# Performance work log

Measured on AMD Instinct MI355X. Metric: run time of the kernel, lower is better.

Reference implementation:

```python
import jax, jax.numpy as jnp
import numpy as np

N_EMBD = 384
HEAD_SIZE = 64
BLOCK_SIZE = 256

def setup_inputs() -> dict:
    key = jax.random.key(0)
    kx, kk, kq, kv = jax.random.split(key, 4)
    bound = 1.0 / np.sqrt(N_EMBD)  # torch nn.Linear default init
    return {
        "x": jax.random.normal(kx, (512, 256, N_EMBD), dtype=jnp.float32),
        "Wk": jax.random.uniform(kk, (N_EMBD, HEAD_SIZE), jnp.float32, -bound, bound),
        "Wq": jax.random.uniform(kq, (N_EMBD, HEAD_SIZE), jnp.float32, -bound, bound),
        "Wv": jax.random.uniform(kv, (N_EMBD, HEAD_SIZE), jnp.float32, -bound, bound),
    }

def reference(x, Wk, Wq, Wv):
    # x: [B, T, C]; single causal self-attention head (eval mode: dropout off)
    B, T, C = x.shape
    k = jnp.einsum('btc,ch->bth', x, Wk)   # [B, T, H]
    q = jnp.einsum('btc,ch->bth', x, Wq)
    v = jnp.einsum('btc,ch->bth', x, Wv)
    scale = 1.0 / jnp.sqrt(jnp.asarray(k.shape[-1], dtype=x.dtype))
    wei = jnp.einsum('bth,bsh->bts', q, k) * scale  # [B, T, T]
    causal = jnp.tril(jnp.ones((T, T), dtype=bool))
    wei = jnp.where(causal, wei, -jnp.inf)
    wei = jax.nn.softmax(wei, axis=-1)
    return jnp.einsum('bts,bsh->bth', wei, v)  # [B, T, H]
```

## Files before the change

### kernel.cpp

```cpp
#include <hip/hip_runtime.h>

#define T_DIM 256
#define C_DIM 384
#define H_DIM 64

typedef __attribute__((ext_vector_type(4))) float f32x4;
typedef __attribute__((ext_vector_type(8))) short bf16x8;
typedef unsigned short u16;

__device__ __forceinline__ u16 f2b(float f) {
  unsigned u = __float_as_uint(f);
  u = (u + 0x7FFFu + ((u >> 16) & 1u)) >> 16;
  return (u16)u;
}
__device__ __forceinline__ unsigned pkbf(float a, float b) {
  unsigned r;
  asm("v_cvt_pk_bf16_f32 %0, %1, %2" : "=v"(r) : "v"(a), "v"(b));
  return r;
}

__device__ __forceinline__ int sw64(int r, int c)  { return r * 64  + (c ^ ((r & 7) << 3)); }
__device__ __forceinline__ int sw256(int h, int t) { return h * 256 + (t ^ ((h & 7) << 3)); }
__device__ __forceinline__ int sw32(int r, int c)  { return r * 32  + (c ^ (((r >> 1) & 3) << 3)); }

__global__ __launch_bounds__(1024, 4)
void head_fused(const float* __restrict__ x,
                const float* __restrict__ Wk,
                const float* __restrict__ Wq,
                const float* __restrict__ Wv,
                float* __restrict__ out)
{
  __shared__ u16 sh[32768];
  u16* xs  = sh;
  u16* wsT = sh + 8192;
  u16* ks  = sh;
  u16* vT  = sh + 16384;

  const int tid  = threadIdx.x;
  const int wv   = tid >> 6;
  const int lane = tid & 63;
  const int g    = lane >> 4;
  const int lr   = lane & 15;
  const int b    = blockIdx.x;

  const float* xb = x + (size_t)b * (T_DIM * C_DIM);

  int xr[2], xc[2];
#pragma unroll
  for (int it = 0; it < 2; ++it) {
    int idx = tid + it * 1024;
    xr[it] = idx >> 3;
    xc[it] = (idx & 7) * 4;
  }
  int wrow[2], wcc[2];
  const float* wsrc[2];
  bool wok[2];
#pragma unroll
  for (int it = 0; it < 2; ++it) {
    int idx = tid + it * 1024;
    wok[it] = (idx < 1536);
    int q   = (idx >> 5) & 63;
    int cc  = idx & 31;
    int seg = q >> 4;
    int hq  = q & 15;
    wrow[it] = seg * 64 + hq * 4;
    wcc[it]  = cc;
    wsrc[it] = ((seg == 0) ? Wq : (seg == 1) ? Wk : Wv) + hq * 4;
  }

  f32x4 acc[12];
#pragma unroll
  for (int nj = 0; nj < 12; ++nj)
    acc[nj] = (f32x4){0.f, 0.f, 0.f, 0.f};

  f32x4 px[2], pwv[2];
#pragma unroll
  for (int it = 0; it < 2; ++it)
    px[it] = *reinterpret_cast<const f32x4*>(xb + xr[it] * C_DIM + xc[it]);
#pragma unroll
  for (int it = 0; it < 2; ++it)
    if (wok[it])
      pwv[it] = *reinterpret_cast<const f32x4*>(wsrc[it] + wcc[it] * H_DIM);

  for (int kt = 0; kt < 12; ++kt) {
    __syncthreads();
#pragma unroll
    for (int it = 0; it < 2; ++it) {
      uint2 pv;
      pv.x = pkbf(px[it][0], px[it][1]);
      pv.y = pkbf(px[it][2], px[it][3]);
      *reinterpret_cast<uint2*>(&xs[sw32(xr[it], xc[it])]) = pv;
    }
#pragma unroll
    for (int it = 0; it < 2; ++it)
      if (wok[it]) {
        wsT[sw32(wrow[it] + 0, wcc[it])] = f2b(pwv[it][0]);
        wsT[sw32(wrow[it] + 1, wcc[it])] = f2b(pwv[it][1]);
        wsT[sw32(wrow[it] + 2, wcc[it])] = f2b(pwv[it][2]);
        wsT[sw32(wrow[it] + 3, wcc[it])] = f2b(pwv[it][3]);
      }
    if (kt < 11) {
      int kk = (kt + 1) * 32;
#pragma unroll
      for (int it = 0; it < 2; ++it)
        px[it] = *reinterpret_cast<const f32x4*>(xb + xr[it] * C_DIM + kk + xc[it]);
#pragma unroll
      for (int it = 0; it < 2; ++it)
        if (wok[it])
          pwv[it] = *reinterpret_cast<const f32x4*>(wsrc[it] + (kk + wcc[it]) * H_DIM);
    }
    __syncthreads();

    bf16x8 afr = *reinterpret_cast<const bf16x8*>(&xs[sw32(wv * 16 + lr, g * 8)]);
#pragma unroll
    for (int nj = 0; nj < 12; ++nj) {
      bf16x8 bfr = *reinterpret_cast<const bf16x8*>(&wsT[sw32(nj * 16 + lr, g * 8)]);
      acc[nj] = __builtin_amdgcn_mfma_f32_16x16x32_bf16(afr, bfr, acc[nj], 0, 0, 0);
    }
  }

  __syncthreads();

  u16* slab = sh + wv * 1024;
#pragma unroll
  for (int nj = 0; nj < 4; ++nj)
#pragma unroll
    for (int e = 0; e < 4; ++e)
      slab[sw64(g * 4 + e, nj * 16 + lr)] = f2b(acc[nj][e]);
  asm volatile("s_waitcnt lgkmcnt(0)" ::: "memory");

  bf16x8 qf[2];
#pragma unroll
  for (int kb = 0; kb < 2; ++kb)
    qf[kb] = *reinterpret_cast<const bf16x8*>(&slab[sw64(lr, kb * 32 + g * 8)]);
  __syncthreads();

#pragma unroll
  for (int nj = 4; nj < 12; ++nj)
#pragma unroll
    for (int e = 0; e < 4; ++e) {
      int r = wv * 16 + g * 4 + e;
      int n = nj * 16 + lr;
      u16 val = f2b(acc[nj][e]);
      if (n < 128) ks[sw64(r, n - 64)] = val;
      else         vT[sw256(n - 128, r)] = val;
    }
  __syncthreads();

  const int r0   = wv * 16;
  const int jmax = wv >> 2;

  f32x4 o[4];
  float m_run = -__builtin_inff(), l_run = 0.f;
#pragma unroll
  for (int nh = 0; nh < 4; ++nh) o[nh] = (f32x4){0.f, 0.f, 0.f, 0.f};

  for (int j = 0; j <= jmax; ++j) {
    f32x4 sT[4];
#pragma unroll
    for (int ni = 0; ni < 4; ++ni) sT[ni] = (f32x4){0.f, 0.f, 0.f, 0.f};
#pragma unroll
    for (int kb = 0; kb < 2; ++kb) {
#pragma unroll
      for (int ni = 0; ni < 4; ++ni) {
        bf16x8 kf = *reinterpret_cast<const bf16x8*>(&ks[sw64(j * 64 + ni * 16 + lr, kb * 32 + g * 8)]);
        sT[ni] = __builtin_amdgcn_mfma_f32_16x16x32_bf16(kf, qf[kb], sT[ni], 0, 0, 0);
      }
    }

    const int q = r0 + lr;
    float pm = -__builtin_inff();
#pragma unroll
    for (int ni = 0; ni < 4; ++ni)
#pragma unroll
      for (int e = 0; e < 4; ++e) {
        float v = sT[ni][e] * 0.125f;
        int kv = j * 64 + ni * 16 + g * 4 + e;
        v = (kv > q) ? -__builtin_inff() : v;
        sT[ni][e] = v;
        pm = fmaxf(pm, v);
      }
    pm = fmaxf(pm, __shfl_xor(pm, 16));
    pm = fmaxf(pm, __shfl_xor(pm, 32));

    float mn = fmaxf(m_run, pm);
    float alpha = __expf(m_run - mn);
    m_run = mn;
    float rs = 0.f;
#pragma unroll
    for (int ni = 0; ni < 4; ++ni)
#pragma unroll
      for (int e = 0; e < 4; ++e) {
        float p = __expf(sT[ni][e] - mn);
        sT[ni][e] = p;
        rs += p;
      }
    rs += __shfl_xor(rs, 16);
    rs += __shfl_xor(rs, 32);
    l_run = l_run * alpha + rs;

#pragma unroll
    for (int e = 0; e < 4; ++e) {
      float am = __shfl(alpha, g * 4 + e);
#pragma unroll
      for (int nh = 0; nh < 4; ++nh) o[nh][e] *= am;
    }

    union PA { unsigned w[4]; bf16x8 v; };
    PA pa[2];
    unsigned pk[4][2];
#pragma unroll
    for (int ni = 0; ni < 4; ++ni) {
      pk[ni][0] = pkbf(sT[ni][0], sT[ni][1]);
      pk[ni][1] = pkbf(sT[ni][2], sT[ni][3]);
    }
#pragma unroll
    for (int kb = 0; kb < 2; ++kb)
#pragma unroll
      for (int w = 0; w < 4; ++w) {
        int sl = ((2 * g + (w >> 1)) & 3) * 16 + lr;
        unsigned lo = __shfl(pk[2 * kb + 0][w & 1], sl);
        unsigned hi = __shfl(pk[2 * kb + 1][w & 1], sl);
        pa[kb].w[w] = (g >= 2) ? hi : lo;
      }

#pragma unroll
    for (int kb = 0; kb < 2; ++kb) {
#pragma unroll
      for (int nh = 0; nh < 4; ++nh) {
        bf16x8 vf = *reinterpret_cast<const bf16x8*>(&vT[sw256(nh * 16 + lr, j * 64 + kb * 32 + g * 8)]);
        o[nh] = __builtin_amdgcn_mfma_f32_16x16x32_bf16(pa[kb].v, vf, o[nh], 0, 0, 0);
      }
    }
  }

  float* ob = out + (size_t)b * (T_DIM * H_DIM);
  float linv[4];
#pragma unroll
  for (int e = 0; e < 4; ++e)
    linv[e] = 1.f / __shfl(l_run, g * 4 + e);
#pragma unroll
  for (int nh = 0; nh < 4; ++nh)
#pragma unroll
    for (int e = 0; e < 4; ++e) {
      int r = r0 + g * 4 + e;
      int h = nh * 16 + lr;
      ob[r * H_DIM + h] = o[nh][e] * linv[e];
    }
}

extern "C" void kernel_launch(void* const* d_in, const int* in_sizes, int n_in,
                              void* d_out, int out_size, void* d_ws, size_t ws_size,
                              hipStream_t stream) {
  const float* x  = (const float*)d_in[0];
  const float* Wk = (const float*)d_in[1];
  const float* Wq = (const float*)d_in[2];
  const float* Wv = (const float*)d_in[3];
  float* out = (float*)d_out;
  int B = in_sizes[0] / (T_DIM * C_DIM);
  head_fused<<<dim3(B), dim3(1024), 0, stream>>>(x, Wk, Wq, Wv, out);
}
```

Measured before the change: 59.65 us.

## Load x fragments directly into registers and widen projection k-step to 64

```diff
diff --git a/kernel.cpp b/kernel.cpp
--- a/kernel.cpp
+++ b/kernel.cpp
@@ -21,7 +21,6 @@
 
 __device__ __forceinline__ int sw64(int r, int c)  { return r * 64  + (c ^ ((r & 7) << 3)); }
 __device__ __forceinline__ int sw256(int h, int t) { return h * 256 + (t ^ ((h & 7) << 3)); }
-__device__ __forceinline__ int sw32(int r, int c)  { return r * 32  + (c ^ (((r >> 1) & 3) << 3)); }
 
 __global__ __launch_bounds__(1024, 4)
 void head_fused(const float* __restrict__ x,
@@ -31,8 +30,7 @@
                 float* __restrict__ out)
 {
   __shared__ u16 sh[32768];
-  u16* xs  = sh;
-  u16* wsT = sh + 8192;
+  u16* wsT = sh;
   u16* ks  = sh;
   u16* vT  = sh + 16384;
 
@@ -44,78 +42,78 @@
   const int b    = blockIdx.x;
 
   const float* xb = x + (size_t)b * (T_DIM * C_DIM);
-
-  int xr[2], xc[2];
-#pragma unroll
-  for (int it = 0; it < 2; ++it) {
-    int idx = tid + it * 1024;
-    xr[it] = idx >> 3;
-    xc[it] = (idx & 7) * 4;
-  }
-  int wrow[2], wcc[2];
-  const float* wsrc[2];
-  bool wok[2];
-#pragma unroll
-  for (int it = 0; it < 2; ++it) {
-    int idx = tid + it * 1024;
-    wok[it] = (idx < 1536);
-    int q   = (idx >> 5) & 63;
-    int cc  = idx & 31;
-    int seg = q >> 4;
-    int hq  = q & 15;
-    wrow[it] = seg * 64 + hq * 4;
-    wcc[it]  = cc;
-    wsrc[it] = ((seg == 0) ? Wq : (seg == 1) ? Wk : Wv) + hq * 4;
-  }
+  const float* xrow = xb + (wv * 16 + lr) * C_DIM + g * 8;
+
+  const float* wsrc[3];
+#pragma unroll
+  for (int it = 0; it < 3; ++it) {
+    const float* W = (it == 0) ? Wq : (it == 1) ? Wk : Wv;
+    wsrc[it] = W + (size_t)lane * H_DIM + wv * 4;
+  }
+  const int wrow0 = wv * 4;
 
   f32x4 acc[12];
 #pragma unroll
   for (int nj = 0; nj < 12; ++nj)
     acc[nj] = (f32x4){0.f, 0.f, 0.f, 0.f};
 
-  f32x4 px[2], pwv[2];
-#pragma unroll
-  for (int it = 0; it < 2; ++it)
-    px[it] = *reinterpret_cast<const f32x4*>(xb + xr[it] * C_DIM + xc[it]);
-#pragma unroll
-  for (int it = 0; it < 2; ++it)
-    if (wok[it])
-      pwv[it] = *reinterpret_cast<const f32x4*>(wsrc[it] + wcc[it] * H_DIM);
-
-  for (int kt = 0; kt < 12; ++kt) {
+  f32x4 pA[2][4];
+  f32x4 pwv[3];
+#pragma unroll
+  for (int c = 0; c < 2; ++c) {
+    const float* p = xrow + c * 64;
+    pA[c][0] = *reinterpret_cast<const f32x4*>(p);
+    pA[c][1] = *reinterpret_cast<const f32x4*>(p + 4);
+    pA[c][2] = *reinterpret_cast<const f32x4*>(p + 32);
+    pA[c][3] = *reinterpret_cast<const f32x4*>(p + 36);
+  }
+#pragma unroll
+  for (int it = 0; it < 3; ++it)
+    pwv[it] = *reinterpret_cast<const f32x4*>(wsrc[it]);
+
+#pragma unroll
+  for (int kt = 0; kt < 6; ++kt) {
+    const int c = kt & 1;
+    bf16x8 afr[2];
+    {
+      union { unsigned w[4]; bf16x8 v; } u0, u1;
+      u0.w[0] = pkbf(pA[c][0][0], pA[c][0][1]);
+      u0.w[1] = pkbf(pA[c][0][2], pA[c][0][3]);
+      u0.w[2] = pkbf(pA[c][1][0], pA[c][1][1]);
+      u0.w[3] = pkbf(pA[c][1][2], pA[c][1][3]);
+      u1.w[0] = pkbf(pA[c][2][0], pA[c][2][1]);
+      u1.w[1] = pkbf(pA[c][2][2], pA[c][2][3]);
+      u1.w[2] = pkbf(pA[c][3][0], pA[c][3][1]);
+      u1.w[3] = pkbf(pA[c][3][2], pA[c][3][3]);
+      afr[0] = u0.v; afr[1] = u1.v;
+    }
+    if (kt < 4) {
+      const float* p = xrow + (kt + 2) * 64;
+      pA[c][0] = *reinterpret_cast<const f32x4*>(p);
+      pA[c][1] = *reinterpret_cast<const f32x4*>(p + 4);
+      pA[c][2] = *reinterpret_cast<const f32x4*>(p + 32);
+      pA[c][3] = *reinterpret_cast<const f32x4*>(p + 36);
+    }
+
     __syncthreads();
 #pragma unroll
-    for (int it = 0; it < 2; ++it) {
-      uint2 pv;
-      pv.x = pkbf(px[it][0], px[it][1]);
-      pv.y = pkbf(px[it][2], px[it][3]);
-      *reinterpret_cast<uint2*>(&xs[sw32(xr[it], xc[it])]) = pv;
-    }
-#pragma unroll
-    for (int it = 0; it < 2; ++it)
-      if (wok[it]) {
-        wsT[sw32(wrow[it] + 0, wcc[it])] = f2b(pwv[it][0]);
-        wsT[sw32(wrow[it] + 1, wcc[it])] = f2b(pwv[it][1]);
-        wsT[sw32(wrow[it] + 2, wcc[it])] = f2b(pwv[it][2]);
-        wsT[sw32(wrow[it] + 3, wcc[it])] = f2b(pwv[it][3]);
-      }
-    if (kt < 11) {
-      int kk = (kt + 1) * 32;
-#pragma unroll
-      for (int it = 0; it < 2; ++it)
-        px[it] = *reinterpret_cast<const f32x4*>(xb + xr[it] * C_DIM + kk + xc[it]);
-#pragma unroll
-      for (int it = 0; it < 2; ++it)
-        if (wok[it])
-          pwv[it] = *reinterpret_cast<const f32x4*>(wsrc[it] + (kk + wcc[it]) * H_DIM);
+    for (int it = 0; it < 3; ++it)
+#pragma unroll
+      for (int jj = 0; jj < 4; ++jj)
+        wsT[sw64(it * 64 + wrow0 + jj, lane)] = f2b(pwv[it][jj]);
+    if (kt < 5) {
+#pragma unroll
+      for (int it = 0; it < 3; ++it)
+        pwv[it] = *reinterpret_cast<const f32x4*>(wsrc[it] + (size_t)(kt + 1) * 64 * H_DIM);
     }
     __syncthreads();
 
-    bf16x8 afr = *reinterpret_cast<const bf16x8*>(&xs[sw32(wv * 16 + lr, g * 8)]);
 #pragma unroll
     for (int nj = 0; nj < 12; ++nj) {
-      bf16x8 bfr = *reinterpret_cast<const bf16x8*>(&wsT[sw32(nj * 16 + lr, g * 8)]);
-      acc[nj] = __builtin_amdgcn_mfma_f32_16x16x32_bf16(afr, bfr, acc[nj], 0, 0, 0);
+      bf16x8 bfr0 = *reinterpret_cast<const bf16x8*>(&wsT[sw64(nj * 16 + lr, g * 8)]);
+      acc[nj] = __builtin_amdgcn_mfma_f32_16x16x32_bf16(afr[0], bfr0, acc[nj], 0, 0, 0);
+      bf16x8 bfr1 = *reinterpret_cast<const bf16x8*>(&wsT[sw64(nj * 16 + lr, 32 + g * 8)]);
+      acc[nj] = __builtin_amdgcn_mfma_f32_16x16x32_bf16(afr[1], bfr1, acc[nj], 0, 0, 0);
     }
   }
 
```

Measured after the change: 92.59 us. 1.55x slower.

## Split fused head into QKV projection and attention kernels via workspace

Applied to the files above, without the earlier changes.

```diff
diff --git a/kernel.cpp b/kernel.cpp
--- a/kernel.cpp
+++ b/kernel.cpp
@@ -22,6 +22,287 @@
 __device__ __forceinline__ int sw64(int r, int c)  { return r * 64  + (c ^ ((r & 7) << 3)); }
 __device__ __forceinline__ int sw256(int h, int t) { return h * 256 + (t ^ ((h & 7) << 3)); }
 __device__ __forceinline__ int sw32(int r, int c)  { return r * 32  + (c ^ (((r >> 1) & 3) << 3)); }
+
+__global__ __launch_bounds__(1024)
+void qkv_k(const float* __restrict__ x,
+           const float* __restrict__ Wk,
+           const float* __restrict__ Wq,
+           const float* __restrict__ Wv,
+           u16* __restrict__ qkv, int b0)
+{
+  __shared__ u16 sh[16384];
+  u16* xs  = sh;
+  u16* wsT = sh + 8192;
+
+  const int tid  = threadIdx.x;
+  const int wv   = tid >> 6;
+  const int lane = tid & 63;
+  const int g    = lane >> 4;
+  const int lr   = lane & 15;
+  const int b    = b0 + blockIdx.x;
+
+  const float* xb = x + (size_t)b * (T_DIM * C_DIM);
+
+  int xr[2], xc[2];
+#pragma unroll
+  for (int it = 0; it < 2; ++it) {
+    int idx = tid + it * 1024;
+    xr[it] = idx >> 3;
+    xc[it] = (idx & 7) * 4;
+  }
+  int wrow[2], wcc[2];
+  const float* wsrc[2];
+  bool wok[2];
+#pragma unroll
+  for (int it = 0; it < 2; ++it) {
+    int idx = tid + it * 1024;
+    wok[it] = (idx < 1536);
+    int q   = (idx >> 5) & 63;
+    int cc  = idx & 31;
+    int seg = q >> 4;
+    int hq  = q & 15;
+    wrow[it] = seg * 64 + hq * 4;
+    wcc[it]  = cc;
+    wsrc[it] = ((seg == 0) ? Wq : (seg == 1) ? Wk : Wv) + hq * 4;
+  }
+
+  f32x4 acc[12];
+#pragma unroll
+  for (int nj = 0; nj < 12; ++nj)
+    acc[nj] = (f32x4){0.f, 0.f, 0.f, 0.f};
+
+  f32x4 px[2], pwv[2];
+#pragma unroll
+  for (int it = 0; it < 2; ++it)
+    px[it] = *reinterpret_cast<const f32x4*>(xb + xr[it] * C_DIM + xc[it]);
+#pragma unroll
+  for (int it = 0; it < 2; ++it)
+    if (wok[it])
+      pwv[it] = *reinterpret_cast<const f32x4*>(wsrc[it] + wcc[it] * H_DIM);
+
+  for (int kt = 0; kt < 12; ++kt) {
+    __syncthreads();
+#pragma unroll
+    for (int it = 0; it < 2; ++it) {
+      uint2 pv;
+      pv.x = pkbf(px[it][0], px[it][1]);
+      pv.y = pkbf(px[it][2], px[it][3]);
+      *reinterpret_cast<uint2*>(&xs[sw32(xr[it], xc[it])]) = pv;
+    }
+#pragma unroll
+    for (int it = 0; it < 2; ++it)
+      if (wok[it]) {
+        wsT[sw32(wrow[it] + 0, wcc[it])] = f2b(pwv[it][0]);
+        wsT[sw32(wrow[it] + 1, wcc[it])] = f2b(pwv[it][1]);
+        wsT[sw32(wrow[it] + 2, wcc[it])] = f2b(pwv[it][2]);
+        wsT[sw32(wrow[it] + 3, wcc[it])] = f2b(pwv[it][3]);
+      }
+    if (kt < 11) {
+      int kk = (kt + 1) * 32;
+#pragma unroll
+      for (int it = 0; it < 2; ++it)
+        px[it] = *reinterpret_cast<const f32x4*>(xb + xr[it] * C_DIM + kk + xc[it]);
+#pragma unroll
+      for (int it = 0; it < 2; ++it)
+        if (wok[it])
+          pwv[it] = *reinterpret_cast<const f32x4*>(wsrc[it] + (kk + wcc[it]) * H_DIM);
+    }
+    __syncthreads();
+
+    bf16x8 afr = *reinterpret_cast<const bf16x8*>(&xs[sw32(wv * 16 + lr, g * 8)]);
+#pragma unroll
+    for (int nj = 0; nj < 12; ++nj) {
+      bf16x8 bfr = *reinterpret_cast<const bf16x8*>(&wsT[sw32(nj * 16 + lr, g * 8)]);
+      acc[nj] = __builtin_amdgcn_mfma_f32_16x16x32_bf16(afr, bfr, acc[nj], 0, 0, 0);
+    }
+  }
+
+  u16* qb = qkv + (size_t)b * 49152;
+  u16* kb = qb + 16384;
+  u16* vb = qb + 32768;
+  const int r0 = wv * 16 + g * 4;
+#pragma unroll
+  for (int nj = 0; nj < 4; ++nj)
+#pragma unroll
+    for (int e = 0; e < 4; ++e)
+      qb[(r0 + e) * 64 + nj * 16 + lr] = f2b(acc[nj][e]);
+#pragma unroll
+  for (int nj = 4; nj < 8; ++nj)
+#pragma unroll
+    for (int e = 0; e < 4; ++e)
+      kb[(r0 + e) * 64 + (nj - 4) * 16 + lr] = f2b(acc[nj][e]);
+#pragma unroll
+  for (int nj = 8; nj < 12; ++nj) {
+    uint2 pv;
+    pv.x = pkbf(acc[nj][0], acc[nj][1]);
+    pv.y = pkbf(acc[nj][2], acc[nj][3]);
+    *reinterpret_cast<uint2*>(&vb[((nj - 8) * 16 + lr) * 256 + r0]) = pv;
+  }
+}
+
+__global__ __launch_bounds__(512, 2)
+void attn_k(const u16* __restrict__ qkv, float* __restrict__ out, int b0)
+{
+  __shared__ u16 sh[32768];
+  u16* ks = sh;
+  u16* vT = sh + 16384;
+
+  const int tid  = threadIdx.x;
+  const int wv   = tid >> 6;
+  const int lane = tid & 63;
+  const int g    = lane >> 4;
+  const int lr   = lane & 15;
+  const int b    = b0 + blockIdx.x;
+
+  const u16* qb = qkv + (size_t)b * 49152;
+  const u16* kg = qb + 16384;
+  const u16* vg = qb + 32768;
+
+#pragma unroll
+  for (int it = 0; it < 4; ++it) {
+    int idx = tid + it * 512;
+    int r = idx >> 3, c = (idx & 7) * 8;
+    *reinterpret_cast<uint4*>(&ks[sw64(r, c)]) =
+        *reinterpret_cast<const uint4*>(&kg[r * 64 + c]);
+  }
+#pragma unroll
+  for (int it = 0; it < 4; ++it) {
+    int idx = tid + it * 512;
+    int h = idx >> 5, t = (idx & 31) * 8;
+    *reinterpret_cast<uint4*>(&vT[sw256(h, t)]) =
+        *reinterpret_cast<const uint4*>(&vg[h * 256 + t]);
+  }
+  bf16x8 qf[2][2];
+#pragma unroll
+  for (int mi = 0; mi < 2; ++mi)
+#pragma unroll
+    for (int kb = 0; kb < 2; ++kb)
+      qf[mi][kb] = *reinterpret_cast<const bf16x8*>(
+          &qb[(wv * 32 + mi * 16 + lr) * 64 + kb * 32 + g * 8]);
+  __syncthreads();
+
+  const int r0   = wv * 32;
+  const int jmax = wv >> 1;
+
+  f32x4 o[2][4];
+  float m_run[2], l_run[2];
+#pragma unroll
+  for (int mi = 0; mi < 2; ++mi) {
+    m_run[mi] = -__builtin_inff();
+    l_run[mi] = 0.f;
+#pragma unroll
+    for (int nh = 0; nh < 4; ++nh) o[mi][nh] = (f32x4){0.f, 0.f, 0.f, 0.f};
+  }
+
+  for (int j = 0; j <= jmax; ++j) {
+    f32x4 sT[2][4];
+#pragma unroll
+    for (int mi = 0; mi < 2; ++mi)
+#pragma unroll
+      for (int ni = 0; ni < 4; ++ni)
+        sT[mi][ni] = (f32x4){0.f, 0.f, 0.f, 0.f};
+#pragma unroll
+    for (int kb = 0; kb < 2; ++kb) {
+#pragma unroll
+      for (int ni = 0; ni < 4; ++ni) {
+        bf16x8 kf = *reinterpret_cast<const bf16x8*>(&ks[sw64(j * 64 + ni * 16 + lr, kb * 32 + g * 8)]);
+#pragma unroll
+        for (int mi = 0; mi < 2; ++mi)
+          sT[mi][ni] = __builtin_amdgcn_mfma_f32_16x16x32_bf16(kf, qf[mi][kb], sT[mi][ni], 0, 0, 0);
+      }
+    }
+
+#pragma unroll
+    for (int mi = 0; mi < 2; ++mi) {
+      const int q = r0 + mi * 16 + lr;
+      float pm = -__builtin_inff();
+#pragma unroll
+      for (int ni = 0; ni < 4; ++ni)
+#pragma unroll
+        for (int e = 0; e < 4; ++e) {
+          float v = sT[mi][ni][e] * 0.125f;
+          int kv = j * 64 + ni * 16 + g * 4 + e;
+          v = (kv > q) ? -__builtin_inff() : v;
+          sT[mi][ni][e] = v;
+          pm = fmaxf(pm, v);
+        }
+      pm = fmaxf(pm, __shfl_xor(pm, 16));
+      pm = fmaxf(pm, __shfl_xor(pm, 32));
+
+      float mn = fmaxf(m_run[mi], pm);
+      float alpha = __expf(m_run[mi] - mn);
+      m_run[mi] = mn;
+      float rs = 0.f;
+#pragma unroll
+      for (int ni = 0; ni < 4; ++ni)
+#pragma unroll
+        for (int e = 0; e < 4; ++e) {
+          float p = __expf(sT[mi][ni][e] - mn);
+          sT[mi][ni][e] = p;
+          rs += p;
+        }
+      rs += __shfl_xor(rs, 16);
+      rs += __shfl_xor(rs, 32);
+      l_run[mi] = l_run[mi] * alpha + rs;
+
+#pragma unroll
+      for (int e = 0; e < 4; ++e) {
+        float am = __shfl(alpha, g * 4 + e);
+#pragma unroll
+        for (int nh = 0; nh < 4; ++nh) o[mi][nh][e] *= am;
+      }
+    }
+
+    union PA { unsigned w[4]; bf16x8 v; };
+    PA pa[2][2];
+#pragma unroll
+    for (int mi = 0; mi < 2; ++mi) {
+      unsigned pk[4][2];
+#pragma unroll
+      for (int ni = 0; ni < 4; ++ni) {
+        pk[ni][0] = pkbf(sT[mi][ni][0], sT[mi][ni][1]);
+        pk[ni][1] = pkbf(sT[mi][ni][2], sT[mi][ni][3]);
+      }
+#pragma unroll
+      for (int kb = 0; kb < 2; ++kb)
+#pragma unroll
+        for (int w = 0; w < 4; ++w) {
+          int sl = ((2 * g + (w >> 1)) & 3) * 16 + lr;
+          unsigned lo = __shfl(pk[2 * kb + 0][w & 1], sl);
+          unsigned hi = __shfl(pk[2 * kb + 1][w & 1], sl);
+          pa[mi][kb].w[w] = (g >= 2) ? hi : lo;
+        }
+    }
+
+#pragma unroll
+    for (int kb = 0; kb < 2; ++kb) {
+#pragma unroll
+      for (int nh = 0; nh < 4; ++nh) {
+        bf16x8 vf = *reinterpret_cast<const bf16x8*>(&vT[sw256(nh * 16 + lr, j * 64 + kb * 32 + g * 8)]);
+#pragma unroll
+        for (int mi = 0; mi < 2; ++mi)
+          o[mi][nh] = __builtin_amdgcn_mfma_f32_16x16x32_bf16(pa[mi][kb].v, vf, o[mi][nh], 0, 0, 0);
+      }
+    }
+  }
+
+  float* ob = out + (size_t)b * (T_DIM * H_DIM);
+#pragma unroll
+  for (int mi = 0; mi < 2; ++mi) {
+    float linv[4];
+#pragma unroll
+    for (int e = 0; e < 4; ++e)
+      linv[e] = 1.f / __shfl(l_run[mi], g * 4 + e);
+#pragma unroll
+    for (int nh = 0; nh < 4; ++nh)
+#pragma unroll
+      for (int e = 0; e < 4; ++e) {
+        int r = r0 + mi * 16 + g * 4 + e;
+        int h = nh * 16 + lr;
+        ob[r * H_DIM + h] = o[mi][nh][e] * linv[e];
+      }
+  }
+}
 
 __global__ __launch_bounds__(1024, 4)
 void head_fused(const float* __restrict__ x,
@@ -120,7 +401,6 @@
   }
 
   __syncthreads();
-
   u16* slab = sh + wv * 1024;
 #pragma unroll
   for (int nj = 0; nj < 4; ++nj)
@@ -258,5 +538,18 @@
   const float* Wv = (const float*)d_in[3];
   float* out = (float*)d_out;
   int B = in_sizes[0] / (T_DIM * C_DIM);
-  head_fused<<<dim3(B), dim3(1024), 0, stream>>>(x, Wk, Wq, Wv, out);
+
+  const size_t per_b = 49152 * sizeof(u16);
+  if (ws_size >= 128 * per_b) {
+    int slice = B;
+    while ((size_t)slice * per_b > ws_size) slice >>= 1;
+    u16* qkv = (u16*)d_ws;
+    for (int b0 = 0; b0 < B; b0 += slice) {
+      int n = (B - b0 < slice) ? (B - b0) : slice;
+      qkv_k<<<dim3(n), dim3(1024), 0, stream>>>(x, Wk, Wq, Wv, qkv, b0);
+      attn_k<<<dim3(n), dim3(512), 0, stream>>>(qkv, out, b0);
+    }
+  } else {
+    head_fused<<<dim3(B), dim3(1024), 0, stream>>>(x, Wk, Wq, Wv, out);
+  }
 }
```

After: 85.67 us. 43.6% more time.
